# Optimization experiments

Hardware: AMD Instinct MI355X
Metric: run time of the kernel (lower is better)

Reference implementation:

```python
import jax, jax.numpy as jnp
import numpy as np

BATCH = 2048
K = 64          # num_clusters
D = 128         # latent_dim / cluster_dim
R1 = 1024
OUT_LEN = 512   # output_length
IN_LEN = 512    # input_length
MIN_CLAMP = 0.0


def setup_inputs() -> dict:
    key = jax.random.key(0)
    k1, k2, k3, k4, k5, k6 = jax.random.split(key, 6)
    z = jax.random.normal(k1, (BATCH, 1, D), dtype=jnp.float32)
    u = jax.random.normal(k2, (BATCH, 1, R1), dtype=jnp.float32)
    member = jax.random.uniform(k3, (BATCH, 1, K), dtype=jnp.float32)
    # parameters
    mu = jax.random.uniform(k4, (K, D), dtype=jnp.float32)  # 1 * torch.rand
    sigma_inv = 10.0 * jnp.broadcast_to(jnp.eye(D, dtype=jnp.float32), (K, D, D))  # zeros with diag 10
    # nn.Linear default init: U(-1/sqrt(fan_in), 1/sqrt(fan_in)), weight shape (out, in)
    bound = 1.0 / np.sqrt(R1)
    W_con = jax.random.uniform(k5, (K, OUT_LEN, R1), dtype=jnp.float32, minval=-bound, maxval=bound)
    W_recon = jax.random.uniform(k6, (K, IN_LEN, R1), dtype=jnp.float32, minval=-bound, maxval=bound)
    return {"z": z, "u": u, "member": member, "mu": mu, "sigma_inv": sigma_inv,
            "W_con": W_con, "W_recon": W_recon}


def _compute_psi(z, mu, sigma_inv):
    # z: (B,1,D), mu: (K,D) -> d: (B,K,D)
    d = mu[None, :, :] - z
    # S = sigma_inv @ sigma_inv^T per cluster: (K,D,D)
    S = jnp.einsum('kde,kfe->kdf', sigma_inv, sigma_inv)
    # Mahalanobis: d^T S d per (b,k)
    d2 = jnp.einsum('bkd,kde,bke->bk', d, S, d)
    d2 = jnp.maximum(d2, MIN_CLAMP)
    psi = jax.nn.softmax(-d2, axis=1)  # (B,K)
    return psi


def reference(z, u, member, mu, sigma_inv, W_con, W_recon):
    psi = _compute_psi(z, mu, sigma_inv)          # (B,K)
    u2 = u[:, 0, :]                                # (B,R1)
    # grouped GEMM + abs: per-cluster |Linear(u)|
    y_LLM = jnp.abs(jnp.einsum('bi,koi->bko', u2, W_con))    # (B,K,OUT_LEN)
    x_LLM = jnp.abs(jnp.einsum('bi,koi->bko', u2, W_recon))  # (B,K,IN_LEN)
    mem = member[:, 0, :]                          # (B,K)
    y_con = jnp.einsum('bk,bko->bo', psi, y_LLM)[:, None, :]   # (B,1,OUT_LEN)
    x_recon = jnp.einsum('bk,bko->bo', mem, x_LLM)[:, None, :]  # (B,1,IN_LEN)
    return (y_con, x_recon)
```

## Files before the change

### kernel.cpp

```cpp
#include <hip/hip_runtime.h>
#include <hip/hip_bf16.h>
#include <stdint.h>

typedef __bf16 bf16_t;
typedef __bf16 bf16x8 __attribute__((ext_vector_type(8)));
typedef __bf16 bf16x4 __attribute__((ext_vector_type(4)));
typedef float  v4f    __attribute__((ext_vector_type(4)));
typedef float  f32x4  __attribute__((ext_vector_type(4)));

#define GLDS16(gp, lp)                                                         \
  __builtin_amdgcn_global_load_lds(                                            \
      (__attribute__((address_space(1))) void*)(gp),                           \
      (__attribute__((address_space(3))) void*)(lp), 16, 0, 0)

#define BATCH 2048
#define KEXP  64
#define NOUT  512
#define R1    1024

__global__ __launch_bounds__(256) void cast_u_k(const float* __restrict__ u,
                                                bf16_t* __restrict__ ub) {
  int idx = blockIdx.x * 256 + threadIdx.x;
  float4 v = ((const float4*)u)[idx];
  bf16x4 o;
  o.x = (bf16_t)v.x; o.y = (bf16_t)v.y; o.z = (bf16_t)v.z; o.w = (bf16_t)v.w;
  ((bf16x4*)ub)[idx] = o;
}

__global__ __launch_bounds__(256) void cast_w_k(const float* __restrict__ wcon,
                                                const float* __restrict__ wrec,
                                                bf16_t* __restrict__ wb) {
  const size_t tid = (size_t)blockIdx.x * 256 + threadIdx.x;
#pragma unroll
  for (int it = 0; it < 8; ++it) {
    size_t idx = tid + (size_t)it * (8192u * 256u);
    size_t e = idx << 2;
    int k = (int)(e >> 20);
    int n = (int)((e >> 10) & 1023);
    int i = (int)(e & 1023);
    const float* src = (n < NOUT)
        ? (wcon + (((size_t)k * NOUT + n) << 10) + i)
        : (wrec + (((size_t)k * NOUT + (n - NOUT)) << 10) + i);
    f32x4 v = __builtin_nontemporal_load((const f32x4*)src);
    bf16x4 o;
    o.x = (bf16_t)v.x; o.y = (bf16_t)v.y; o.z = (bf16_t)v.z; o.w = (bf16_t)v.w;
    ((bf16x4*)wb)[idx] = o;
  }
}

__global__ __launch_bounds__(256) void psi_d2_k(const float* __restrict__ z,
                                                const float* __restrict__ mu,
                                                const float* __restrict__ sig,
                                                float* __restrict__ d2g) {
  __shared__ float dv[64][132];
  __shared__ float Ss[16][128];
  const int t = threadIdx.x;
  const int k = blockIdx.x;
  const int b0 = blockIdx.y * 64;

  const float* muk = mu + k * 128;
#pragma unroll
  for (int i = 0; i < 8; ++i) {
    int f4 = i * 256 + t;
    int row = f4 >> 5, c4 = f4 & 31;
    float4 zq = ((const float4*)(z + (size_t)(b0 + row) * 128))[c4];
    float4 mq = ((const float4*)muk)[c4];
    float4 dq;
    dq.x = mq.x - zq.x; dq.y = mq.y - zq.y;
    dq.z = mq.z - zq.z; dq.w = mq.w - zq.w;
    *(float4*)&dv[row][c4 * 4] = dq;
  }

  const int et = t & 15, bt = t >> 4;
  const float* Sk = sig + ((size_t)k << 14);
  float acc[4][8];
#pragma unroll
  for (int j = 0; j < 4; ++j)
#pragma unroll
    for (int i = 0; i < 8; ++i) acc[j][i] = 0.f;

  for (int dblk = 0; dblk < 8; ++dblk) {
    __syncthreads();
#pragma unroll
    for (int i = 0; i < 2; ++i) {
      int f4 = i * 256 + t;
      int row = f4 >> 5, c4 = f4 & 31;
      *(float4*)&Ss[row][c4 * 4] =
          ((const float4*)(Sk + (size_t)(dblk * 16 + row) * 128))[c4];
    }
    __syncthreads();

#pragma unroll
    for (int d4 = 0; d4 < 4; ++d4) {
      float4 a[4];
#pragma unroll
      for (int j = 0; j < 4; ++j)
        a[j] = *(const float4*)&dv[bt * 4 + j][dblk * 16 + d4 * 4];
#pragma unroll
      for (int dd = 0; dd < 4; ++dd) {
        float4 s0 = *(const float4*)&Ss[d4 * 4 + dd][et * 8];
        float4 s1 = *(const float4*)&Ss[d4 * 4 + dd][et * 8 + 4];
        float av[4] = {a[0][dd], a[1][dd], a[2][dd], a[3][dd]};
#pragma unroll
        for (int j = 0; j < 4; ++j) {
          acc[j][0] = fmaf(s0.x, av[j], acc[j][0]);
          acc[j][1] = fmaf(s0.y, av[j], acc[j][1]);
          acc[j][2] = fmaf(s0.z, av[j], acc[j][2]);
          acc[j][3] = fmaf(s0.w, av[j], acc[j][3]);
          acc[j][4] = fmaf(s1.x, av[j], acc[j][4]);
          acc[j][5] = fmaf(s1.y, av[j], acc[j][5]);
          acc[j][6] = fmaf(s1.z, av[j], acc[j][6]);
          acc[j][7] = fmaf(s1.w, av[j], acc[j][7]);
        }
      }
    }
  }

  float v2[4];
#pragma unroll
  for (int j = 0; j < 4; ++j) {
    float s = 0.f;
#pragma unroll
    for (int i = 0; i < 8; ++i) s = fmaf(acc[j][i], acc[j][i], s);
    v2[j] = s;
  }
#pragma unroll
  for (int j = 0; j < 4; ++j) {
    v2[j] += __shfl_xor(v2[j], 1);
    v2[j] += __shfl_xor(v2[j], 2);
    v2[j] += __shfl_xor(v2[j], 4);
    v2[j] += __shfl_xor(v2[j], 8);
  }
  if (et == 0) {
#pragma unroll
    for (int j = 0; j < 4; ++j)
      d2g[(size_t)(b0 + bt * 4 + j) * 64 + k] = v2[j];
  }
}

__global__ __launch_bounds__(256) void psi_sm_k(const float* __restrict__ d2g,
                                                float* __restrict__ psi) {
  const int b = blockIdx.x * 4 + (threadIdx.x >> 6);
  const int lane = threadIdx.x & 63;
  float x = fmaxf(d2g[(size_t)b * 64 + lane], 0.0f);
  float m = x;
  m = fminf(m, __shfl_xor(m, 1));  m = fminf(m, __shfl_xor(m, 2));
  m = fminf(m, __shfl_xor(m, 4));  m = fminf(m, __shfl_xor(m, 8));
  m = fminf(m, __shfl_xor(m, 16)); m = fminf(m, __shfl_xor(m, 32));
  float ex = __expf(m - x);
  float s = ex;
  s += __shfl_xor(s, 1);  s += __shfl_xor(s, 2);  s += __shfl_xor(s, 4);
  s += __shfl_xor(s, 8);  s += __shfl_xor(s, 16); s += __shfl_xor(s, 32);
  psi[(size_t)b * 64 + lane] = ex / s;
}

__global__ __launch_bounds__(256, 2)
void fused_gemm(const bf16_t* __restrict__ ub,
                const bf16_t* __restrict__ wb,
                const float* __restrict__ psi,
                const float* __restrict__ member,
                float* __restrict__ out) {
  __shared__ bf16_t Alds[128 * 64];
  __shared__ bf16_t Blds[128 * 64];
  __shared__ float wlds[128];

  const int t = threadIdx.x, lane = t & 63, wv = t >> 6;
  const int bm0 = blockIdx.x * 128;
  const int n0  = blockIdx.y * 128;
  const int e0  = blockIdx.z * 8;
  const bool is_y = (n0 < NOUT);
  const float* wsel = is_y ? psi : member;
  const int wm = wv & 1, wn = wv >> 1;
  const int l15 = lane & 15, quad = lane >> 4;

  v4f acc[4][4], oacc[4][4];
#pragma unroll
  for (int mi = 0; mi < 4; ++mi)
#pragma unroll
    for (int ni = 0; ni < 4; ++ni)
#pragma unroll
      for (int r = 0; r < 4; ++r) { acc[mi][ni][r] = 0.f; oacc[mi][ni][r] = 0.f; }

  const int rA = wv * 8 + (lane >> 3);
  const int c8 = (((lane & 7) ^ (lane >> 3)) * 8);
  const bf16_t* au  = ub + (size_t)(bm0 + rA) * R1 + c8;
  const bf16_t* bw0 = wb + (size_t)(n0 + rA) * R1 + c8;

  const int fsw = l15 & 7;

  for (int ke = 0; ke < 8; ++ke) {
    const int ex = e0 + ke;
    const bf16_t* bw = bw0 + ((size_t)ex << 20);
    for (int kk = 0; kk < R1; kk += 64) {
      __syncthreads();
      if (kk == 0 && t < 128) wlds[t] = wsel[(size_t)(bm0 + t) * 64 + ex];
#pragma unroll
      for (int j = 0; j < 4; ++j) {
        GLDS16(au + (size_t)(j * 32) * R1 + kk, &Alds[(j * 32 + wv * 8) * 64]);
        GLDS16(bw + (size_t)(j * 32) * R1 + kk, &Blds[(j * 32 + wv * 8) * 64]);
      }
      __syncthreads();

      const bf16_t* Ab = &Alds[(wm * 64 + l15) * 64];
      const bf16_t* Bb = &Blds[(wn * 64 + l15) * 64];
#pragma unroll
      for (int ks = 0; ks < 2; ++ks) {
        const int co = ((ks * 4 + quad) ^ fsw) * 8;
        bf16x8 af[4], bfr[4];
#pragma unroll
        for (int i = 0; i < 4; ++i) {
          af[i]  = *(const bf16x8*)(Ab + i * 16 * 64 + co);
          bfr[i] = *(const bf16x8*)(Bb + i * 16 * 64 + co);
        }
#pragma unroll
        for (int mi = 0; mi < 4; ++mi)
#pragma unroll
          for (int ni = 0; ni < 4; ++ni)
            acc[mi][ni] = __builtin_amdgcn_mfma_f32_16x16x32_bf16(
                af[mi], bfr[ni], acc[mi][ni], 0, 0, 0);
      }
    }
#pragma unroll
    for (int mi = 0; mi < 4; ++mi) {
      float wr[4];
#pragma unroll
      for (int r = 0; r < 4; ++r) wr[r] = wlds[wm * 64 + mi * 16 + quad * 4 + r];
#pragma unroll
      for (int ni = 0; ni < 4; ++ni)
#pragma unroll
        for (int r = 0; r < 4; ++r) {
          oacc[mi][ni][r] += fabsf(acc[mi][ni][r]) * wr[r];
          acc[mi][ni][r] = 0.f;
        }
    }
  }

  float* obase = is_y ? out : out + (size_t)BATCH * NOUT;
  const int oc = (is_y ? n0 : n0 - NOUT) + wn * 64 + l15;
#pragma unroll
  for (int mi = 0; mi < 4; ++mi)
#pragma unroll
    for (int ni = 0; ni < 4; ++ni)
#pragma unroll
      for (int r = 0; r < 4; ++r) {
        int brow = bm0 + wm * 64 + mi * 16 + quad * 4 + r;
        atomicAdd(&obase[(size_t)brow * NOUT + oc + ni * 16], oacc[mi][ni][r]);
      }
}

extern "C" void kernel_launch(void* const* d_in, const int* in_sizes, int n_in,
                              void* d_out, int out_size, void* d_ws, size_t ws_size,
                              hipStream_t stream) {
  const float* z    = (const float*)d_in[0];
  const float* u    = (const float*)d_in[1];
  const float* mem  = (const float*)d_in[2];
  const float* mu   = (const float*)d_in[3];
  const float* sig  = (const float*)d_in[4];
  const float* wcon = (const float*)d_in[5];
  const float* wrec = (const float*)d_in[6];
  float* out = (float*)d_out;

  char* ws = (char*)d_ws;
  bf16_t* ub  = (bf16_t*)ws;
  bf16_t* wb  = (bf16_t*)(ws + ((size_t)4 << 20));
  float*  psw = (float*)(ws + ((size_t)132 << 20));
  float*  d2g = (float*)(ws + ((size_t)132 << 20) + ((size_t)512 << 10));

  hipMemsetAsync(d_out, 0, (size_t)out_size * sizeof(float), stream);
  cast_u_k<<<2048, 256, 0, stream>>>(u, ub);
  cast_w_k<<<8192, 256, 0, stream>>>(wcon, wrec, wb);
  psi_d2_k<<<dim3(64, 32), 256, 0, stream>>>(z, mu, sig, d2g);
  psi_sm_k<<<512, 256, 0, stream>>>(d2g, psw);
  fused_gemm<<<dim3(16, 8, 8), 256, 0, stream>>>(ub, wb, psw, mem, out);
}
```

Measured before the change: 677.0 us.

## Switch GEMM to 32x32x16 MFMA, preload weights, simplify weight cast kernel

The fused grouped GEMM moves from 16x16x32 to 32x32x16 bf16 MFMA tiles, reorganizing the accumulator layout, LDS fragment reads and swizzle. This cuts LDS fragment loads per MFMA. The per-expert weights (psi/member) for all 8 experts are now preloaded into LDS once at kernel start instead of on each expert's first k-step. Separately, the weight cast kernel drops its 8-iteration loop and nontemporal loads in favour of one vector per thread with 8x more blocks.

```diff
diff --git a/kernel.cpp b/kernel.cpp
--- a/kernel.cpp
+++ b/kernel.cpp
@@ -5,8 +5,7 @@
 typedef __bf16 bf16_t;
 typedef __bf16 bf16x8 __attribute__((ext_vector_type(8)));
 typedef __bf16 bf16x4 __attribute__((ext_vector_type(4)));
-typedef float  v4f    __attribute__((ext_vector_type(4)));
-typedef float  f32x4  __attribute__((ext_vector_type(4)));
+typedef float  v16f   __attribute__((ext_vector_type(16)));
 
 #define GLDS16(gp, lp)                                                         \
   __builtin_amdgcn_global_load_lds(                                            \
@@ -30,22 +29,18 @@
 __global__ __launch_bounds__(256) void cast_w_k(const float* __restrict__ wcon,
                                                 const float* __restrict__ wrec,
                                                 bf16_t* __restrict__ wb) {
-  const size_t tid = (size_t)blockIdx.x * 256 + threadIdx.x;
-#pragma unroll
-  for (int it = 0; it < 8; ++it) {
-    size_t idx = tid + (size_t)it * (8192u * 256u);
-    size_t e = idx << 2;
-    int k = (int)(e >> 20);
-    int n = (int)((e >> 10) & 1023);
-    int i = (int)(e & 1023);
-    const float* src = (n < NOUT)
-        ? (wcon + (((size_t)k * NOUT + n) << 10) + i)
-        : (wrec + (((size_t)k * NOUT + (n - NOUT)) << 10) + i);
-    f32x4 v = __builtin_nontemporal_load((const f32x4*)src);
-    bf16x4 o;
-    o.x = (bf16_t)v.x; o.y = (bf16_t)v.y; o.z = (bf16_t)v.z; o.w = (bf16_t)v.w;
-    ((bf16x4*)wb)[idx] = o;
-  }
+  size_t idx = (size_t)blockIdx.x * 256 + threadIdx.x;
+  size_t e = idx << 2;
+  int k = (int)(e >> 20);
+  int n = (int)((e >> 10) & 1023);
+  int i = (int)(e & 1023);
+  const float* src = (n < NOUT)
+      ? (wcon + (((size_t)k * NOUT + n) << 10) + i)
+      : (wrec + (((size_t)k * NOUT + (n - NOUT)) << 10) + i);
+  float4 v = *(const float4*)src;
+  bf16x4 o;
+  o.x = (bf16_t)v.x; o.y = (bf16_t)v.y; o.z = (bf16_t)v.z; o.w = (bf16_t)v.w;
+  ((bf16x4*)wb)[idx] = o;
 }
 
 __global__ __launch_bounds__(256) void psi_d2_k(const float* __restrict__ z,
@@ -162,7 +157,7 @@
                 float* __restrict__ out) {
   __shared__ bf16_t Alds[128 * 64];
   __shared__ bf16_t Blds[128 * 64];
-  __shared__ float wlds[128];
+  __shared__ float wlds[8 * 128];
 
   const int t = threadIdx.x, lane = t & 63, wv = t >> 6;
   const int bm0 = blockIdx.x * 128;
@@ -171,29 +166,38 @@
   const bool is_y = (n0 < NOUT);
   const float* wsel = is_y ? psi : member;
   const int wm = wv & 1, wn = wv >> 1;
-  const int l15 = lane & 15, quad = lane >> 4;
-
-  v4f acc[4][4], oacc[4][4];
-#pragma unroll
-  for (int mi = 0; mi < 4; ++mi)
-#pragma unroll
-    for (int ni = 0; ni < 4; ++ni)
-#pragma unroll
-      for (int r = 0; r < 4; ++r) { acc[mi][ni][r] = 0.f; oacc[mi][ni][r] = 0.f; }
+  const int l31 = lane & 31, half = lane >> 5, l7 = lane & 7;
+
+#pragma unroll
+  for (int i = 0; i < 4; ++i) {
+    int f = i * 256 + t;
+    wlds[f] = wsel[(size_t)(bm0 + (f & 127)) * 64 + (e0 + (f >> 7))];
+  }
+
+  v16f acc[2][2], oacc[2][2];
+#pragma unroll
+  for (int mi = 0; mi < 2; ++mi)
+#pragma unroll
+    for (int ni = 0; ni < 2; ++ni)
+#pragma unroll
+      for (int r = 0; r < 16; ++r) { acc[mi][ni][r] = 0.f; oacc[mi][ni][r] = 0.f; }
 
   const int rA = wv * 8 + (lane >> 3);
   const int c8 = (((lane & 7) ^ (lane >> 3)) * 8);
   const bf16_t* au  = ub + (size_t)(bm0 + rA) * R1 + c8;
   const bf16_t* bw0 = wb + (size_t)(n0 + rA) * R1 + c8;
 
-  const int fsw = l15 & 7;
+  int row32[16];
+#pragma unroll
+  for (int r = 0; r < 16; ++r) row32[r] = (r & 3) + 8 * (r >> 2) + 4 * half;
+
+  const bf16_t* Ab = &Alds[(wm * 64 + l31) * 64];
+  const bf16_t* Bb = &Blds[(wn * 64 + l31) * 64];
 
   for (int ke = 0; ke < 8; ++ke) {
-    const int ex = e0 + ke;
-    const bf16_t* bw = bw0 + ((size_t)ex << 20);
+    const bf16_t* bw = bw0 + ((size_t)(e0 + ke) << 20);
     for (int kk = 0; kk < R1; kk += 64) {
       __syncthreads();
-      if (kk == 0 && t < 128) wlds[t] = wsel[(size_t)(bm0 + t) * 64 + ex];
 #pragma unroll
       for (int j = 0; j < 4; ++j) {
         GLDS16(au + (size_t)(j * 32) * R1 + kk, &Alds[(j * 32 + wv * 8) * 64]);
@@ -201,34 +205,33 @@
       }
       __syncthreads();
 
-      const bf16_t* Ab = &Alds[(wm * 64 + l15) * 64];
-      const bf16_t* Bb = &Blds[(wn * 64 + l15) * 64];
-#pragma unroll
-      for (int ks = 0; ks < 2; ++ks) {
-        const int co = ((ks * 4 + quad) ^ fsw) * 8;
-        bf16x8 af[4], bfr[4];
-#pragma unroll
-        for (int i = 0; i < 4; ++i) {
-          af[i]  = *(const bf16x8*)(Ab + i * 16 * 64 + co);
-          bfr[i] = *(const bf16x8*)(Bb + i * 16 * 64 + co);
+#pragma unroll
+      for (int ks = 0; ks < 4; ++ks) {
+        const int co = (((ks * 2 + half) ^ l7)) * 8;
+        bf16x8 af[2], bfr[2];
+#pragma unroll
+        for (int i = 0; i < 2; ++i) {
+          af[i]  = *(const bf16x8*)(Ab + i * 32 * 64 + co);
+          bfr[i] = *(const bf16x8*)(Bb + i * 32 * 64 + co);
         }
 #pragma unroll
-        for (int mi = 0; mi < 4; ++mi)
-#pragma unroll
-          for (int ni = 0; ni < 4; ++ni)
-            acc[mi][ni] = __builtin_amdgcn_mfma_f32_16x16x32_bf16(
+        for (int mi = 0; mi < 2; ++mi)
+#pragma unroll
+          for (int ni = 0; ni < 2; ++ni)
+            acc[mi][ni] = __builtin_amdgcn_mfma_f32_32x32x16_bf16(
                 af[mi], bfr[ni], acc[mi][ni], 0, 0, 0);
       }
     }
 #pragma unroll
-    for (int mi = 0; mi < 4; ++mi) {
-      float wr[4];
-#pragma unroll
-      for (int r = 0; r < 4; ++r) wr[r] = wlds[wm * 64 + mi * 16 + quad * 4 + r];
-#pragma unroll
-      for (int ni = 0; ni < 4; ++ni)
-#pragma unroll
-        for (int r = 0; r < 4; ++r) {
+    for (int mi = 0; mi < 2; ++mi) {
+      float wr[16];
+#pragma unroll
+      for (int r = 0; r < 16; ++r)
+        wr[r] = wlds[ke * 128 + wm * 64 + mi * 32 + row32[r]];
+#pragma unroll
+      for (int ni = 0; ni < 2; ++ni)
+#pragma unroll
+        for (int r = 0; r < 16; ++r) {
           oacc[mi][ni][r] += fabsf(acc[mi][ni][r]) * wr[r];
           acc[mi][ni][r] = 0.f;
         }
@@ -236,15 +239,15 @@
   }
 
   float* obase = is_y ? out : out + (size_t)BATCH * NOUT;
-  const int oc = (is_y ? n0 : n0 - NOUT) + wn * 64 + l15;
-#pragma unroll
-  for (int mi = 0; mi < 4; ++mi)
-#pragma unroll
-    for (int ni = 0; ni < 4; ++ni)
-#pragma unroll
-      for (int r = 0; r < 4; ++r) {
-        int brow = bm0 + wm * 64 + mi * 16 + quad * 4 + r;
-        atomicAdd(&obase[(size_t)brow * NOUT + oc + ni * 16], oacc[mi][ni][r]);
+  const int oc0 = (is_y ? n0 : n0 - NOUT) + wn * 64 + l31;
+#pragma unroll
+  for (int mi = 0; mi < 2; ++mi)
+#pragma unroll
+    for (int ni = 0; ni < 2; ++ni)
+#pragma unroll
+      for (int r = 0; r < 16; ++r) {
+        int brow = bm0 + wm * 64 + mi * 32 + row32[r];
+        atomicAdd(&obase[(size_t)brow * NOUT + oc0 + ni * 32], oacc[mi][ni][r]);
       }
 }
 
@@ -268,7 +271,7 @@
 
   hipMemsetAsync(d_out, 0, (size_t)out_size * sizeof(float), stream);
   cast_u_k<<<2048, 256, 0, stream>>>(u, ub);
-  cast_w_k<<<8192, 256, 0, stream>>>(wcon, wrec, wb);
+  cast_w_k<<<65536, 256, 0, stream>>>(wcon, wrec, wb);
   psi_d2_k<<<dim3(64, 32), 256, 0, stream>>>(z, mu, sig, d2g);
   psi_sm_k<<<512, 256, 0, stream>>>(d2g, psw);
   fused_gemm<<<dim3(16, 8, 8), 256, 0, stream>>>(ub, wb, psw, mem, out);
```

After: 713.7 us. 1.05x slower.
